# Performance work log

Hardware: AMD Instinct MI355X
Metric: run time of the kernel (lower is better)

Reference implementation:

```python
import jax, jax.numpy as jnp
import numpy as np

N_HEAD = 16
HEAD_SIZE = 64  # n_embd // n_head = 1024 // 16


def setup_inputs() -> dict:
    key = jax.random.key(0)
    k1, k2 = jax.random.split(key)
    B, T, C = 2, 2048, 1024
    x = jax.random.normal(k1, (B, T, C), dtype=jnp.float32)
    w_attn = jax.random.normal(k2, (C, 3 * C), dtype=jnp.float32) * (C ** -0.5)
    b_attn = jnp.zeros((3 * C,), dtype=jnp.float32)
    return {"x": x, "w_attn": w_attn, "b_attn": b_attn}


def reference(x, w_attn, b_attn):
    B, T, C = x.shape
    qkv = x @ w_attn + b_attn  # [B, T, 3C]
    q, k, v = jnp.split(qkv, 3, axis=-1)
    # [B, T, H, D] -> [B, H, T, D]
    def heads(t):
        return t.reshape(B, T, N_HEAD, HEAD_SIZE).transpose(0, 2, 1, 3)
    q, k, v = heads(q), heads(k), heads(v)
    scale = HEAD_SIZE ** -0.5
    wei = jnp.einsum('bhqd,bhkd->bhqk', q, k) * scale  # [B, H, T, T]
    causal = jnp.tril(jnp.ones((T, T), dtype=bool))
    wei = jnp.where(causal, wei, -jnp.inf)
    wei = jax.nn.softmax(wei, axis=-1)
    out = jnp.einsum('bhqk,bhkd->bhqd', wei, v)  # [B, H, T, D]
    out = out.transpose(0, 2, 1, 3).reshape(B, T, C)
    return out
```

## Files before the change

### kernel.cpp

```cpp
#include <hip/hip_runtime.h>
#include <hip/hip_bf16.h>

#define BSZ 2
#define SEQ 2048
#define CDIM 1024
#define NHEAD 16
#define HDIM 64
#define M_GEMM (BSZ * SEQ)
#define N_GEMM (3 * CDIM)
#define K_GEMM CDIM
#define QK_PITCH (2 * CDIM)

typedef __attribute__((ext_vector_type(8))) short short8;
typedef __attribute__((ext_vector_type(4))) short short4v;
typedef __attribute__((ext_vector_type(4))) float f32x4;

__device__ __forceinline__ short bf16_rn(float f) {
    unsigned u = __builtin_bit_cast(unsigned, f);
    u += 0x7FFF + ((u >> 16) & 1);
    return (short)(u >> 16);
}

__device__ __forceinline__ void gl2lds16(const short* g, short* l) {
    __builtin_amdgcn_global_load_lds(
        (const __attribute__((address_space(1))) unsigned int*)g,
        (__attribute__((address_space(3))) unsigned int*)l, 16, 0, 0);
}

#define WAITV2() asm volatile("s_waitcnt vmcnt(2)")
#define WAITV3() asm volatile("s_waitcnt vmcnt(3)")
#define WAITV0() asm volatile("s_waitcnt vmcnt(0)")
#define LGKM0()  asm volatile("s_waitcnt lgkmcnt(0)")
#define SCB()    __builtin_amdgcn_sched_barrier(0)
#define BARRIER() __builtin_amdgcn_s_barrier()

__global__ __launch_bounds__(256) void cvt_fused(const float* __restrict__ X,
                                                 const float* __restrict__ W,
                                                 short* __restrict__ Xb,
                                                 short* __restrict__ WT) {
    const int tid = threadIdx.x;
    if (blockIdx.x < 2048) {
        size_t idx = ((size_t)blockIdx.x * 256 + tid) * 8;
        float4 a = *(const float4*)&X[idx];
        float4 b = *(const float4*)&X[idx + 4];
        short8 o;
        o[0] = bf16_rn(a.x); o[1] = bf16_rn(a.y); o[2] = bf16_rn(a.z); o[3] = bf16_rn(a.w);
        o[4] = bf16_rn(b.x); o[5] = bf16_rn(b.y); o[6] = bf16_rn(b.z); o[7] = bf16_rn(b.w);
        *(short8*)&Xb[idx] = o;
        return;
    }
    __shared__ short T[64][72];
    const int bid = blockIdx.x - 2048;
    const int n0 = (bid % 48) * 64;
    const int k0 = (bid / 48) * 64;
#pragma unroll
    for (int pass = 0; pass < 4; ++pass) {
        int i = pass * 256 + tid;
        int kr = i >> 4;
        int n4 = i & 15;
        float4 v = *(const float4*)&W[(size_t)(k0 + kr) * N_GEMM + n0 + n4 * 4];
        T[n4 * 4 + 0][kr] = bf16_rn(v.x);
        T[n4 * 4 + 1][kr] = bf16_rn(v.y);
        T[n4 * 4 + 2][kr] = bf16_rn(v.z);
        T[n4 * 4 + 3][kr] = bf16_rn(v.w);
    }
    __syncthreads();
#pragma unroll
    for (int pass = 0; pass < 2; ++pass) {
        int o = pass * 256 + tid;
        int nr = o >> 3;
        int c8 = o & 7;
        *(short8*)&WT[(size_t)(n0 + nr) * K_GEMM + k0 + c8 * 8] =
            *(const short8*)&T[nr][c8 * 8];
    }
}

__global__ __launch_bounds__(512, 2) void qkv_gemm_8ph(const short* __restrict__ A,
                                                       const short* __restrict__ Bt,
                                                       const float* __restrict__ bias,
                                                       short* __restrict__ Yqk,
                                                       short* __restrict__ Yv) {
    __shared__ short Asl[32768];
    __shared__ short Bsl[24576];

    const int tid  = threadIdx.x;
    const int w    = tid >> 6;
    const int lane = tid & 63;
    const int l16  = lane & 15;
    const int quad = lane >> 4;
    const int wm   = w >> 2;
    const int wn   = w & 3;
    const int ls   = lane >> 3;
    const int lc   = lane & 7;
    const int fsw  = l16 & 7;

    const int orig = blockIdx.y * 16 + blockIdx.x;
    const int xcd  = orig & 7;
    const int idx  = orig >> 3;
    const int bM   = ((xcd & 1) << 3) + (idx & 7);
    const int bN   = (xcd >> 1) * 4 + (idx >> 3);
    const int m0   = bM << 8;
    const int n0   = bN * 192;

    const short* Ab = A  + (size_t)m0 * K_GEMM;
    const short* Bb = Bt + (size_t)n0 * K_GEMM;

    f32x4 acc[8][3];
#pragma unroll
    for (int i = 0; i < 8; ++i)
#pragma unroll
        for (int j = 0; j < 3; ++j) acc[i][j] = (f32x4){0.f, 0.f, 0.f, 0.f};

    auto stageA = [&](int unit, int tt, int sbuf) {
#pragma unroll
        for (int i = 0; i < 2; ++i) {
            const int u0 = (i * 8 + w) * 8;
            const int tr = (u0 & 63) + ((u0 >> 6) << 7) + unit * 64;
            gl2lds16(Ab + (size_t)(tr + ls) * K_GEMM + tt * 64 + ((lc ^ ls) << 3),
                     &Asl[sbuf * 16384 + tr * 64]);
        }
    };
    auto stageBE = [&](int tt, int sbuf) {
#pragma unroll
        for (int i = 0; i < 2; ++i) {
            const int jb = i * 64 + w * 8;
            const int gr = (jb >> 5) * 48 + (jb & 31);
            gl2lds16(Bb + (size_t)(gr + ls) * K_GEMM + tt * 64 + ((lc ^ ls) << 3),
                     &Bsl[sbuf * 12288 + jb * 64]);
        }
    };
    auto stageBO = [&](int tt, int sbuf) {
        const int t8 = w * 8;
        const int jb = 128 + t8;
        const int gr = (t8 >> 4) * 48 + 32 + (t8 & 15);
        gl2lds16(Bb + (size_t)(gr + ls) * K_GEMM + tt * 64 + ((lc ^ ls) << 3),
                 &Bsl[sbuf * 12288 + jb * 64]);
    };
    auto rdA = [&](int ab, int mi, int ks) -> short8 {
        const int r = wm * 128 + mi * 16 + l16;
        return *(const short8*)&Asl[ab + r * 64 + ((ks * 4 + quad) ^ fsw) * 8];
    };
    auto rdB = [&](int bb, int ni, int ks) -> short8 {
        const int j = (ni < 2) ? (wn * 32 + ni * 16 + l16)
                               : (128 + wn * 16 + l16);
        return *(const short8*)&Bsl[bb + j * 64 + ((ks * 4 + quad) ^ fsw) * 8];
    };

    stageA(0, 0, 0);
    stageBE(0, 0);
    stageA(1, 0, 0);
    stageBO(0, 0);
    WAITV3();
    SCB(); BARRIER(); SCB();

    for (int t = 0; t < 16; ++t) {
        const int buf = t & 1;
        const int sb  = buf ^ 1;
        const int tn  = (t + 1) & 15;
        const int ab  = buf * 16384;
        const int bb  = buf * 12288;

        short8 Af[4][2], Bf[3][2];

#pragma unroll
        for (int mi = 0; mi < 4; ++mi)
#pragma unroll
            for (int ks = 0; ks < 2; ++ks) Af[mi][ks] = rdA(ab, mi, ks);
#pragma unroll
        for (int ni = 0; ni < 2; ++ni)
#pragma unroll
            for (int ks = 0; ks < 2; ++ks) Bf[ni][ks] = rdB(bb, ni, ks);
        stageA(0, tn, sb);
        SCB(); BARRIER(); LGKM0(); SCB();
        __builtin_amdgcn_s_setprio(1);
#pragma unroll
        for (int mi = 0; mi < 4; ++mi)
#pragma unroll
            for (int ni = 0; ni < 2; ++ni)
#pragma unroll
                for (int ks = 0; ks < 2; ++ks)
                    acc[mi][ni] = __builtin_amdgcn_mfma_f32_16x16x32_bf16(
                        Af[mi][ks], Bf[ni][ks], acc[mi][ni], 0, 0, 0);
        __builtin_amdgcn_s_setprio(0);
        WAITV2();
        SCB(); BARRIER(); SCB();

#pragma unroll
        for (int ks = 0; ks < 2; ++ks) Bf[2][ks] = rdB(bb, 2, ks);
        stageBE(tn, sb);
        SCB(); BARRIER(); LGKM0(); SCB();
        __builtin_amdgcn_s_setprio(1);
#pragma unroll
        for (int mi = 0; mi < 4; ++mi)
#pragma unroll
            for (int ks = 0; ks < 2; ++ks)
                acc[mi][2] = __builtin_amdgcn_mfma_f32_16x16x32_bf16(
                    Af[mi][ks], Bf[2][ks], acc[mi][2], 0, 0, 0);
        __builtin_amdgcn_s_setprio(0);
        SCB(); BARRIER(); SCB();

#pragma unroll
        for (int mi = 0; mi < 4; ++mi)
#pragma unroll
            for (int ks = 0; ks < 2; ++ks) Af[mi][ks] = rdA(ab, 4 + mi, ks);
        stageA(1, tn, sb);
        SCB(); BARRIER(); LGKM0(); SCB();
        __builtin_amdgcn_s_setprio(1);
#pragma unroll
        for (int mi = 0; mi < 4; ++mi)
#pragma unroll
            for (int ni = 0; ni < 2; ++ni)
#pragma unroll
                for (int ks = 0; ks < 2; ++ks)
                    acc[4 + mi][ni] = __builtin_amdgcn_mfma_f32_16x16x32_bf16(
                        Af[mi][ks], Bf[ni][ks], acc[4 + mi][ni], 0, 0, 0);
        __builtin_amdgcn_s_setprio(0);
        SCB(); BARRIER(); SCB();

        stageBO(tn, sb);
        SCB(); BARRIER(); SCB();
        __builtin_amdgcn_s_setprio(1);
#pragma unroll
        for (int mi = 0; mi < 4; ++mi)
#pragma unroll
            for (int ks = 0; ks < 2; ++ks)
                acc[4 + mi][2] = __builtin_amdgcn_mfma_f32_16x16x32_bf16(
                    Af[mi][ks], Bf[2][ks], acc[4 + mi][2], 0, 0, 0);
        __builtin_amdgcn_s_setprio(0);
        WAITV3();
        SCB(); BARRIER(); SCB();
    }
    WAITV0();

    const float log2e8 = 0.125f * 1.44269504f;
#pragma unroll
    for (int mi = 0; mi < 8; ++mi) {
#pragma unroll
        for (int ni = 0; ni < 3; ++ni) {
            const int colg = n0 + wn * 48 + ni * 16 + l16;
            const float bb2 = bias[colg];
            if (colg >= 2 * CDIM) {
                const int row0 = m0 + wm * 128 + mi * 16 + quad * 4;
                short4v pk;
#pragma unroll
                for (int r = 0; r < 4; ++r) pk[r] = bf16_rn(acc[mi][ni][r] + bb2);
                *(short4v*)&Yv[(size_t)(colg - 2 * CDIM) * M_GEMM + row0] = pk;
            } else {
                const float qs = (colg < CDIM) ? log2e8 : 1.0f;
#pragma unroll
                for (int r = 0; r < 4; ++r) {
                    const int row = m0 + wm * 128 + mi * 16 + quad * 4 + r;
                    Yqk[(size_t)row * QK_PITCH + colg] =
                        bf16_rn((acc[mi][ni][r] + bb2) * qs);
                }
            }
        }
    }
}

__global__ __launch_bounds__(512) void attn_mfma(const short* __restrict__ qk,
                                                 const short* __restrict__ vT,
                                                 float* __restrict__ out) {
    const int b = blockIdx.z;
    const int h = blockIdx.y;
    const int bx = blockIdx.x;
    const int tid = threadIdx.x;
    const int w = tid >> 6;
    const int ws = w >> 2;
    const int wq = w & 3;
    const int lane = tid & 63;
    const int quad = lane >> 4;
    const int l16 = lane & 15;

    const int qts   = ws ? (31 - bx) : bx;
    const int ktmax = 31 - bx;
    const int q0 = qts * 64;

    __shared__ short Ks[2][64 * 64];
    __shared__ short Vt[2][64 * 64];

    int koff, voff, ldso;
    {
        const int cid = tid;
        const int row = cid >> 3;
        const int hK = (row & 3) | (((row >> 3) & 1) << 2);
        koff = row * QK_PITCH + (((cid & 7) ^ hK)) * 8;
        voff = row * M_GEMM + (((cid & 7) ^ (row & 7))) * 8;
        ldso = (w * 64) * 8;
    }

    const short* qrow = qk + (size_t)(b * SEQ + q0 + wq * 16 + l16) * QK_PITCH + h * HDIM;
    short8 aq[2];
    aq[0] = *(const short8*)(qrow + quad * 8);
    aq[1] = *(const short8*)(qrow + 32 + quad * 8);

    float l_run = 0.f;
    f32x4 o_acc[4];
#pragma unroll
    for (int dt = 0; dt < 4; ++dt) o_acc[dt] = (f32x4){0.f, 0.f, 0.f, 0.f};

    const int qglob = q0 + wq * 16 + l16;
    const short* kb0 = qk + (size_t)(b * SEQ) * QK_PITCH + CDIM + h * HDIM;
    const short* vb0 = vT + (size_t)(h * HDIM) * M_GEMM + b * SEQ;

    const int ksl = l16 & 7;

    const int Fq = ((l16 >> 2) << 3) + (l16 & 3);

    gl2lds16(kb0 + koff, &Ks[0][ldso]);
    gl2lds16(vb0 + voff, &Vt[0][ldso]);
    __syncthreads();

    for (int kt = 0; kt <= ktmax; ++kt) {
        const int cur = kt & 1;

        if (kt < ktmax) {
            const short* kbase = kb0 + (size_t)(kt + 1) * 64 * QK_PITCH;
            const short* vbase = vb0 + (kt + 1) * 64;
            gl2lds16(kbase + koff, &Ks[cur ^ 1][ldso]);
            gl2lds16(vbase + voff, &Vt[cur ^ 1][ldso]);
        }

        if (kt <= qts) {
            const short* KsC = Ks[cur];
            const short* VtC = Vt[cur];

            f32x4 s[4];
#pragma unroll
            for (int nt = 0; nt < 4; ++nt) s[nt] = (f32x4){0.f, 0.f, 0.f, 0.f};
            __builtin_amdgcn_s_setprio(1);
#pragma unroll
            for (int nt = 0; nt < 4; ++nt) {
                const int F  = (nt >> 1) * 32 + (nt & 1) * 4 + Fq;
                const int hF = (F & 3) | (((F >> 3) & 1) << 2);
#pragma unroll
                for (int ks = 0; ks < 2; ++ks) {
                    short8 kf = *(const short8*)&KsC[F * 64 + (((ks * 4 + quad) ^ hF) * 8)];
                    s[nt] = __builtin_amdgcn_mfma_f32_16x16x32_bf16(kf, aq[ks], s[nt], 0, 0, 0);
                }
            }
            __builtin_amdgcn_s_setprio(0);

            short8 pa0, pa1;
            float lsum = 0.f;
            if (kt < qts) {
#pragma unroll
                for (int nt = 0; nt < 4; ++nt)
#pragma unroll
                    for (int r = 0; r < 4; ++r) {
                        float pp = __builtin_amdgcn_exp2f(s[nt][r]);
                        lsum += pp;
                        short pb = bf16_rn(pp);
                        if (nt < 2) pa0[(nt & 1) * 4 + r] = pb;
                        else        pa1[(nt & 1) * 4 + r] = pb;
                    }
            } else {
#pragma unroll
                for (int nt = 0; nt < 4; ++nt)
#pragma unroll
                    for (int r = 0; r < 4; ++r) {
                        int key = kt * 64 + (nt >> 1) * 32 + quad * 8 + (nt & 1) * 4 + r;
                        float pp = __builtin_amdgcn_exp2f(s[nt][r]);
                        pp = (key > qglob) ? 0.f : pp;
                        lsum += pp;
                        short pb = bf16_rn(pp);
                        if (nt < 2) pa0[(nt & 1) * 4 + r] = pb;
                        else        pa1[(nt & 1) * 4 + r] = pb;
                    }
            }
            l_run += lsum;

            __builtin_amdgcn_s_setprio(1);
#pragma unroll
            for (int dt = 0; dt < 4; ++dt)
#pragma unroll
                for (int ks = 0; ks < 2; ++ks) {
                    short8 bv = *(const short8*)&VtC[(dt * 16 + l16) * 64 +
                                                     ((ks * 4 + quad) ^ ksl) * 8];
                    o_acc[dt] = __builtin_amdgcn_mfma_f32_16x16x32_bf16(
                        ks ? pa1 : pa0, bv, o_acc[dt], 0, 0, 0);
                }
            __builtin_amdgcn_s_setprio(0);
        }

        __syncthreads();
    }

    float l = l_run;
    l += __shfl_xor(l, 16);
    l += __shfl_xor(l, 32);
#pragma unroll
    for (int r = 0; r < 4; ++r) {
        float lq = __shfl(l, quad * 4 + r);
        float inv = 1.f / lq;
        int row = q0 + wq * 16 + quad * 4 + r;
        float* optr = out + (size_t)(b * SEQ + row) * CDIM + h * HDIM;
#pragma unroll
        for (int dt = 0; dt < 4; ++dt)
            optr[dt * 16 + l16] = o_acc[dt][r] * inv;
    }
}

extern "C" void kernel_launch(void* const* d_in, const int* in_sizes, int n_in,
                              void* d_out, int out_size, void* d_ws, size_t ws_size,
                              hipStream_t stream) {
    const float* x      = (const float*)d_in[0];
    const float* w_attn = (const float*)d_in[1];
    const float* b_attn = (const float*)d_in[2];
    float* out = (float*)d_out;

    short* qk  = (short*)d_ws;
    short* vT  = (short*)((char*)d_ws + 16777216);
    short* xb  = (short*)((char*)d_ws + 25165824);
    short* wT  = (short*)((char*)d_ws + 33554432);

    cvt_fused<<<2048 + 768, 256, 0, stream>>>(x, w_attn, xb, wT);

    dim3 g1(N_GEMM / 192, M_GEMM / 256);
    qkv_gemm_8ph<<<g1, 512, 0, stream>>>(xb, wT, b_attn, qk, vT);

    dim3 g2(SEQ / 128, NHEAD, BSZ);
    attn_mfma<<<g2, 512, 0, stream>>>(qk, vT, out);
}
```

Before: 150.7 us.

## Simplify QKV GEMM main loop to one barrier per K-tile with upfront prefetch

Replaces the four-phase interleaved staging schedule in the QKV projection GEMM, which used partial vmcnt waits and several barriers per iteration, with a simpler loop. The loop issues all next-tile global-to-LDS loads at the start, runs two MFMA halves over all three B column groups, then does a full vmcnt(0) wait and a single barrier. This removes most intra-iteration barriers but loses the fine-grained overlap of loads with compute. The full wait at the end may expose memory latency, and more B fragments are kept live in registers.

```diff
diff --git a/kernel.cpp b/kernel.cpp
--- a/kernel.cpp
+++ b/kernel.cpp
@@ -27,8 +27,6 @@
         (__attribute__((address_space(3))) unsigned int*)l, 16, 0, 0);
 }
 
-#define WAITV2() asm volatile("s_waitcnt vmcnt(2)")
-#define WAITV3() asm volatile("s_waitcnt vmcnt(3)")
 #define WAITV0() asm volatile("s_waitcnt vmcnt(0)")
 #define LGKM0()  asm volatile("s_waitcnt lgkmcnt(0)")
 #define SCB()    __builtin_amdgcn_sched_barrier(0)
@@ -150,7 +148,7 @@
     stageBE(0, 0);
     stageA(1, 0, 0);
     stageBO(0, 0);
-    WAITV3();
+    WAITV0();
     SCB(); BARRIER(); SCB();
 
     for (int t = 0; t < 16; ++t) {
@@ -160,6 +158,11 @@
         const int ab  = buf * 16384;
         const int bb  = buf * 12288;
 
+        stageA(0, tn, sb);
+        stageBE(tn, sb);
+        stageA(1, tn, sb);
+        stageBO(tn, sb);
+
         short8 Af[4][2], Bf[3][2];
 
 #pragma unroll
@@ -167,67 +170,38 @@
 #pragma unroll
             for (int ks = 0; ks < 2; ++ks) Af[mi][ks] = rdA(ab, mi, ks);
 #pragma unroll
-        for (int ni = 0; ni < 2; ++ni)
+        for (int ni = 0; ni < 3; ++ni)
 #pragma unroll
             for (int ks = 0; ks < 2; ++ks) Bf[ni][ks] = rdB(bb, ni, ks);
-        stageA(0, tn, sb);
-        SCB(); BARRIER(); LGKM0(); SCB();
+        LGKM0(); SCB();
         __builtin_amdgcn_s_setprio(1);
 #pragma unroll
         for (int mi = 0; mi < 4; ++mi)
 #pragma unroll
-            for (int ni = 0; ni < 2; ++ni)
+            for (int ni = 0; ni < 3; ++ni)
 #pragma unroll
                 for (int ks = 0; ks < 2; ++ks)
                     acc[mi][ni] = __builtin_amdgcn_mfma_f32_16x16x32_bf16(
                         Af[mi][ks], Bf[ni][ks], acc[mi][ni], 0, 0, 0);
         __builtin_amdgcn_s_setprio(0);
-        WAITV2();
-        SCB(); BARRIER(); SCB();
-
-#pragma unroll
-        for (int ks = 0; ks < 2; ++ks) Bf[2][ks] = rdB(bb, 2, ks);
-        stageBE(tn, sb);
-        SCB(); BARRIER(); LGKM0(); SCB();
+
+#pragma unroll
+        for (int mi = 0; mi < 4; ++mi)
+#pragma unroll
+            for (int ks = 0; ks < 2; ++ks) Af[mi][ks] = rdA(ab, 4 + mi, ks);
+        LGKM0(); SCB();
         __builtin_amdgcn_s_setprio(1);
 #pragma unroll
         for (int mi = 0; mi < 4; ++mi)
 #pragma unroll
-            for (int ks = 0; ks < 2; ++ks)
-                acc[mi][2] = __builtin_amdgcn_mfma_f32_16x16x32_bf16(
-                    Af[mi][ks], Bf[2][ks], acc[mi][2], 0, 0, 0);
-        __builtin_amdgcn_s_setprio(0);
-        SCB(); BARRIER(); SCB();
-
-#pragma unroll
-        for (int mi = 0; mi < 4; ++mi)
-#pragma unroll
-            for (int ks = 0; ks < 2; ++ks) Af[mi][ks] = rdA(ab, 4 + mi, ks);
-        stageA(1, tn, sb);
-        SCB(); BARRIER(); LGKM0(); SCB();
-        __builtin_amdgcn_s_setprio(1);
-#pragma unroll
-        for (int mi = 0; mi < 4; ++mi)
-#pragma unroll
-            for (int ni = 0; ni < 2; ++ni)
+            for (int ni = 0; ni < 3; ++ni)
 #pragma unroll
                 for (int ks = 0; ks < 2; ++ks)
                     acc[4 + mi][ni] = __builtin_amdgcn_mfma_f32_16x16x32_bf16(
                         Af[mi][ks], Bf[ni][ks], acc[4 + mi][ni], 0, 0, 0);
         __builtin_amdgcn_s_setprio(0);
-        SCB(); BARRIER(); SCB();
-
-        stageBO(tn, sb);
-        SCB(); BARRIER(); SCB();
-        __builtin_amdgcn_s_setprio(1);
-#pragma unroll
-        for (int mi = 0; mi < 4; ++mi)
-#pragma unroll
-            for (int ks = 0; ks < 2; ++ks)
-                acc[4 + mi][2] = __builtin_amdgcn_mfma_f32_16x16x32_bf16(
-                    Af[mi][ks], Bf[2][ks], acc[4 + mi][2], 0, 0, 0);
-        __builtin_amdgcn_s_setprio(0);
-        WAITV3();
+
+        WAITV0();
         SCB(); BARRIER(); SCB();
     }
     WAITV0();
```

Result: slower. 153.9 us (+2.1%).
